# Kernel optimization log

Hardware: AMD Instinct MI355X
Metric: run time of the kernel (lower is better)

## Reference

```python
import jax, jax.numpy as jnp
import numpy as np

B, T, I, H, O = 64, 512, 64, 1024, 64
STEPS = 49 - 1  # output_len - 1 decode iterations


def _cell(x_t, h, c, Wih, Whh, b):
    # PyTorch LSTM gate order: i, f, g, o
    gates = x_t @ Wih.T + h @ Whh.T + b  # [B, 4H]
    i, f, g, o = jnp.split(gates, 4, axis=-1)
    i = jax.nn.sigmoid(i)
    f = jax.nn.sigmoid(f)
    g = jnp.tanh(g)
    o = jax.nn.sigmoid(o)
    c2 = f * c + i * g
    h2 = o * jnp.tanh(c2)
    return h2, c2


def setup_inputs() -> dict:
    key = jax.random.key(0)
    ks = jax.random.split(key, 12)
    s = 0.05
    return {
        "x": jax.random.normal(ks[0], (B, T, I), jnp.float32),
        "y0": jax.random.normal(ks[1], (B, I), jnp.float32),
        "Wih_e": jax.random.normal(ks[2], (4 * H, I), jnp.float32) * s,
        "Whh_e": jax.random.normal(ks[3], (4 * H, H), jnp.float32) * s,
        "bih_e": jax.random.normal(ks[4], (4 * H,), jnp.float32) * s,
        "bhh_e": jax.random.normal(ks[5], (4 * H,), jnp.float32) * s,
        "Wih_d": jax.random.normal(ks[6], (4 * H, I), jnp.float32) * s,
        "Whh_d": jax.random.normal(ks[7], (4 * H, H), jnp.float32) * s,
        "bih_d": jax.random.normal(ks[8], (4 * H,), jnp.float32) * s,
        "bhh_d": jax.random.normal(ks[9], (4 * H,), jnp.float32) * s,
        "Wfc": jax.random.normal(ks[10], (O, H), jnp.float32) * s,
        "bfc": jax.random.normal(ks[11], (O,), jnp.float32) * s,
    }


def reference(x, y0, Wih_e, Whh_e, bih_e, bhh_e, Wih_d, Whh_d, bih_d, bhh_d, Wfc, bfc):
    b = x.shape[0]
    h0 = jnp.zeros((b, Whh_e.shape[1]), x.dtype)
    c0 = h0

    # Encoder: scan over time (zero initial hidden, as in initHidden)
    be = bih_e + bhh_e

    def enc_step(carry, x_t):
        h, c = carry
        h, c = _cell(x_t, h, c, Wih_e, Whh_e, be)
        return (h, c), None

    (h, c), _ = jax.lax.scan(enc_step, (h0, c0), jnp.swapaxes(x, 0, 1))

    # Decoder: original loop never updates input_decoder -> constant y0 each step.
    bd = bih_d + bhh_d
    xin = y0 @ Wih_d.T + bd  # precompute constant input projection [B, 4H]

    def dec_step(carry, _):
        hd, cd = carry
        gates = xin + hd @ Whh_d.T
        i, f, g, o = jnp.split(gates, 4, axis=-1)
        i = jax.nn.sigmoid(i)
        f = jax.nn.sigmoid(f)
        g = jnp.tanh(g)
        o = jax.nn.sigmoid(o)
        c2 = f * cd + i * g
        h2 = o * jnp.tanh(c2)
        out = h2 @ Wfc.T + bfc  # [B, O]
        return (h2, c2), out

    _, ys = jax.lax.scan(dec_step, (h, c), None, length=STEPS)  # [STEPS, B, O]
    # torch.concat(total, dim=1): step-major along feature axis
    return jnp.swapaxes(ys, 0, 1).reshape(b, STEPS * ys.shape[-1])
```

## Files before the change

### kernel.cpp

```cpp
#include <hip/hip_runtime.h>
#include <hip/hip_fp16.h>

typedef _Float16 f16;
typedef _Float16 f16x8 __attribute__((ext_vector_type(8)));
typedef float f32x16 __attribute__((ext_vector_type(16)));

#define T_N 512
#define DSTEPS 48
#define TOTSTEPS 560
#define NWG 64

#define OFF_WHHE 0ull
#define SZ_WHH   (4096ull*1024*2)
#define OFF_WHHD (OFF_WHHE + SZ_WHH)
#define OFF_WIHE (OFF_WHHD + SZ_WHH)
#define SZ_WIH   (4096ull*64*2)
#define OFF_WIHD (OFF_WIHE + SZ_WIH)
#define OFF_WFC  (OFF_WIHD + SZ_WIH)
#define SZ_WFC   (64ull*1024*2)
#define OFF_XP   (OFF_WFC + SZ_WFC)
#define SZ_XP    (512ull*4096*2)
#define OFF_Y0   (OFF_XP + SZ_XP)
#define SZ_Y0    (4096ull*2)
#define OFF_BE   (OFF_Y0 + SZ_Y0)
#define OFF_BD   (OFF_BE + 4096ull*4)
#define OFF_FLG  (OFF_BD + 4096ull*4)
#define SZ_FLG   (561ull*256*4)
#define OFF_H    ((OFF_FLG + SZ_FLG + 255ull) & ~255ull)

__global__ void prologue(const float* __restrict__ x, const float* __restrict__ y0,
    const float* __restrict__ wihE, const float* __restrict__ whhE,
    const float* __restrict__ bihE, const float* __restrict__ bhhE,
    const float* __restrict__ wihD, const float* __restrict__ whhD,
    const float* __restrict__ bihD, const float* __restrict__ bhhD,
    const float* __restrict__ wfc, char* __restrict__ ws)
{
  const long long gid = (long long)blockIdx.x * 256 + threadIdx.x;
  const long long gsz = (long long)gridDim.x * 256;
  f16* whhEp = (f16*)(ws + OFF_WHHE);
  f16* whhDp = (f16*)(ws + OFF_WHHD);
  f16* wihEp = (f16*)(ws + OFF_WIHE);
  f16* wihDp = (f16*)(ws + OFF_WIHD);
  f16* wfcp  = (f16*)(ws + OFF_WFC);
  f16* xp    = (f16*)(ws + OFF_XP);
  f16* y0p   = (f16*)(ws + OFF_Y0);
  float* be  = (float*)(ws + OFF_BE);
  float* bd  = (float*)(ws + OFF_BD);

  for (long long idx = gid; idx < 4194304ll; idx += gsz) {
    int j = (int)idx & 7, l = (int)(idx >> 3) & 63, kk = (int)(idx >> 9) & 31;
    int i = (int)(idx >> 14) & 1, ks = (int)(idx >> 15) & 1, w = (int)(idx >> 16);
    int nl = i * 32 + (l & 31);
    int grow = (nl >> 4) * 1024 + w * 16 + (nl & 15);
    int k = ks * 512 + kk * 16 + ((l >> 5) << 3) + j;
    whhEp[idx] = (f16)whhE[(long long)grow * 1024 + k];
    whhDp[idx] = (f16)whhD[(long long)grow * 1024 + k];
  }
  for (long long idx = gid; idx < 262144ll; idx += gsz) {
    int j = (int)idx & 7, l = (int)(idx >> 3) & 63, kx = (int)(idx >> 9) & 1;
    int i = (int)(idx >> 10) & 1, ks = (int)(idx >> 11) & 1, w = (int)(idx >> 12);
    int nl = i * 32 + (l & 31);
    int grow = (nl >> 4) * 1024 + w * 16 + (nl & 15);
    int k = (ks * 2 + kx) * 16 + ((l >> 5) << 3) + j;
    wihEp[idx] = (f16)wihE[grow * 64 + k];
    wihDp[idx] = (f16)wihD[grow * 64 + k];
  }
  for (long long idx = gid; idx < 65536ll; idx += gsz) {
    int j = (int)idx & 7, l = (int)(idx >> 3) & 63, kk = (int)(idx >> 9) & 31;
    int i = (int)(idx >> 14) & 1, ks = (int)(idx >> 15) & 1;
    int o = i * 32 + (l & 31);
    int k = ks * 512 + kk * 16 + ((l >> 5) << 3) + j;
    wfcp[idx] = (f16)wfc[o * 1024 + k];
  }
  for (long long idx = gid; idx < 2097152ll; idx += gsz) {
    int kw = (int)idx & 15, b = (int)(idx >> 4) & 63, kkx = (int)(idx >> 10) & 3, t = (int)(idx >> 12);
    xp[idx] = (f16)x[(long long)b * 32768 + t * 64 + kkx * 16 + kw];
  }
  for (long long idx = gid; idx < 4096ll; idx += gsz) {
    int kw = (int)idx & 15, b = (int)(idx >> 4) & 63, kkx = (int)(idx >> 10) & 3;
    y0p[idx] = (f16)y0[b * 64 + kkx * 16 + kw];
  }
  for (long long idx = gid; idx < 4096ll; idx += gsz) {
    be[idx] = bihE[idx] + bhhE[idx];
    bd[idx] = bihD[idx] + bhhD[idx];
  }
}

__device__ __forceinline__ float sigf(float x) { return 1.0f / (1.0f + __expf(-x)); }
__device__ __forceinline__ float tanhfast(float x) {
  x = fminf(fmaxf(x, -15.f), 15.f);
  float e = __expf(2.0f * x);
  return (e - 1.0f) / (e + 1.0f);
}

#define MFMA(a,b,c) __builtin_amdgcn_mfma_f32_32x32x16_f16((a),(b),(c),0,0,0)

__launch_bounds__(256, 1)
__global__ void lstm_persist(char* __restrict__ ws, float* __restrict__ out,
                             const float* __restrict__ bfc)
{
  const int w    = blockIdx.x;
  const int tid  = threadIdx.x;
  const int lane = tid & 63;
  const int wave = tid >> 6;
  const int wm   = wave & 1;
  const int ks   = wave >> 1;

  const f16* whhEp = (const f16*)(ws + OFF_WHHE) + (size_t)w * 65536;
  const f16* whhDp = (const f16*)(ws + OFF_WHHD) + (size_t)w * 65536;
  const f16* wihEp = (const f16*)(ws + OFF_WIHE) + (size_t)w * 4096;
  const f16* wihDp = (const f16*)(ws + OFF_WIHD) + (size_t)w * 4096;
  const f16* wfcp  = (const f16*)(ws + OFF_WFC);
  const f16* xp    = (const f16*)(ws + OFF_XP);
  const f16* y0p   = (const f16*)(ws + OFF_Y0);
  const float* be  = (const float*)(ws + OFF_BE);
  const float* bd  = (const float*)(ws + OFF_BD);
  unsigned* flags  = (unsigned*)(ws + OFF_FLG);
  f16* hb          = (f16*)(ws + OFF_H);

  __shared__ float lds_g[2][64][66];
  __shared__ float bias_s[2][64];
  __shared__ unsigned seen[2];

  if (tid < 64) {
    int g4 = tid >> 4, u = tid & 15;
    bias_s[0][tid] = be[g4 * 1024 + w * 16 + u];
    bias_s[1][tid] = bd[g4 * 1024 + w * 16 + u];
  }
  if (tid < 2) seen[tid] = 0u;

  const int aoff = (wm * 32 + (lane & 31)) * 16 + (lane >> 5) * 8;
  const int boff = lane * 8;
  const int bsel = tid >> 2;
  const int u0   = (tid & 3) * 4;
  const int n0   = lane & 31;

  f16x8 bf0[32], bf1[32];
#pragma unroll
  for (int kk = 0; kk < 32; ++kk) {
    bf0[kk] = *(const f16x8*)(whhEp + (size_t)ks * 32768 + kk * 512 + boff);
    bf1[kk] = *(const f16x8*)(whhEp + (size_t)ks * 32768 + 16384 + kk * 512 + boff);
  }

  float c0 = 0.f, c1 = 0.f, c2 = 0.f, c3 = 0.f;
  __syncthreads();

#pragma unroll 1
  for (int t = 0; t < TOTSTEPS; ++t) {
    const bool enc = (t < T_N);

    if (t == T_N) {
#pragma unroll
      for (int kk = 0; kk < 32; ++kk) {
        bf0[kk] = *(const f16x8*)(whhDp + (size_t)ks * 32768 + kk * 512 + boff);
        bf1[kk] = *(const f16x8*)(whhDp + (size_t)ks * 32768 + 16384 + kk * 512 + boff);
      }
    }

    const f16* xblk = enc ? (xp + (size_t)t * 4096) : y0p;
    const f16* wihp = enc ? wihEp : wihDp;
    f16x8 xa0 = *(const f16x8*)(xblk + (ks * 2 + 0) * 1024 + aoff);
    f16x8 xa1 = *(const f16x8*)(xblk + (ks * 2 + 1) * 1024 + aoff);
    f16x8 wf0 = *(const f16x8*)(wihp + ((ks * 2 + 0) * 2 + 0) * 512 + boff);
    f16x8 wf1 = *(const f16x8*)(wihp + ((ks * 2 + 0) * 2 + 1) * 512 + boff);
    f16x8 wf2 = *(const f16x8*)(wihp + ((ks * 2 + 1) * 2 + 0) * 512 + boff);
    f16x8 wf3 = *(const f16x8*)(wihp + ((ks * 2 + 1) * 2 + 1) * 512 + boff);

    if (t > 0) {
      if (wave < 2) {
        const unsigned* fp = flags + (size_t)t * 256 + wave * 128 + lane;
        int ok;
        do {
          unsigned v0 = __hip_atomic_load(fp,      __ATOMIC_RELAXED, __HIP_MEMORY_SCOPE_AGENT);
          unsigned v1 = __hip_atomic_load(fp + 64, __ATOMIC_RELAXED, __HIP_MEMORY_SCOPE_AGENT);
          ok = __all((v0 == 1u) & (v1 == 1u));
          if (!ok) __builtin_amdgcn_s_sleep(1);
        } while (!ok);
        __hip_atomic_store(&seen[wave], (unsigned)t, __ATOMIC_RELEASE, __HIP_MEMORY_SCOPE_WORKGROUP);
      } else {
        while (__hip_atomic_load(&seen[wm], __ATOMIC_ACQUIRE, __HIP_MEMORY_SCOPE_WORKGROUP) < (unsigned)t)
          ;
      }
      asm volatile("" ::: "memory");
    }

    f16x8 af[32];
    if (t > 0) {
      const f16* hblk = hb + (size_t)(t - 1) * 65536;
#pragma unroll
      for (int kk = 0; kk < 32; ++kk)
        af[kk] = *(const f16x8*)(hblk + (size_t)(ks * 32 + kk) * 1024 + aoff);
    }

    f32x16 acc0, acc1;
#pragma unroll
    for (int i = 0; i < 16; ++i) { acc0[i] = 0.f; acc1[i] = 0.f; }
    acc0 = MFMA(xa0, wf0, acc0); acc0 = MFMA(xa1, wf1, acc0);
    acc1 = MFMA(xa0, wf2, acc1); acc1 = MFMA(xa1, wf3, acc1);

    if (t > 0) {
#pragma unroll
      for (int kk = 0; kk < 32; ++kk) {
        acc0 = MFMA(af[kk], bf0[kk], acc0);
        acc1 = MFMA(af[kk], bf1[kk], acc1);
      }
    }

    {
      const float* bs = enc ? bias_s[0] : bias_s[1];
      const float b0h = 0.5f * bs[n0];
      const float b1h = 0.5f * bs[32 + n0];
#pragma unroll
      for (int i = 0; i < 16; ++i) { acc0[i] += b0h; acc1[i] += b1h; }
    }

    {
      const int mb = wm * 32 + ((lane >> 5) << 2);
#pragma unroll
      for (int r = 0; r < 16; ++r) {
        const int m = mb + (r & 3) + ((r >> 2) << 3);
        lds_g[ks][n0][m]      = acc0[r];
        lds_g[ks][32 + n0][m] = acc1[r];
      }
    }
    __syncthreads();

    union { unsigned long long u64; f16 h4[4]; } hu;
    float cc[4] = {c0, c1, c2, c3};
#pragma unroll
    for (int j = 0; j < 4; ++j) {
      const int u = u0 + j;
      float ig = lds_g[0][u][bsel]      + lds_g[1][u][bsel];
      float fg = lds_g[0][16 + u][bsel] + lds_g[1][16 + u][bsel];
      float gg = lds_g[0][32 + u][bsel] + lds_g[1][32 + u][bsel];
      float og = lds_g[0][48 + u][bsel] + lds_g[1][48 + u][bsel];
      float cn = sigf(fg) * cc[j] + sigf(ig) * tanhfast(gg);
      cc[j] = cn;
      hu.h4[j] = (f16)(sigf(og) * tanhfast(cn));
    }
    c0 = cc[0]; c1 = cc[1]; c2 = cc[2]; c3 = cc[3];

    {
      f16* dst = hb + (size_t)t * 65536 + (size_t)w * 1024 + bsel * 16 + u0;
      unsigned long long addr = (unsigned long long)(size_t)dst;
      asm volatile("global_store_dwordx2 %0, %1, off sc0 sc1" : : "v"(addr), "v"(hu.u64) : "memory");
    }
    asm volatile("s_waitcnt vmcnt(0)" ::: "memory");
    if (lane == 0) {
      unsigned* fa = flags + (size_t)(t + 1) * 256 + wave * 64 + w;
      unsigned long long addr = (unsigned long long)(size_t)fa;
      unsigned one = 1u;
      asm volatile("global_store_dword %0, %1, off sc0 sc1" : : "v"(addr), "v"(one) : "memory");
    }
  }

  if (w < DSTEPS) {
    __syncthreads();
    const int s = T_N + 1 + w;
#pragma unroll
    for (int kk = 0; kk < 32; ++kk) {
      bf0[kk] = *(const f16x8*)(wfcp + (size_t)ks * 32768 + kk * 512 + boff);
      bf1[kk] = *(const f16x8*)(wfcp + (size_t)ks * 32768 + 16384 + kk * 512 + boff);
    }
    if (wave < 2) {
      const unsigned* fp = flags + (size_t)s * 256 + wave * 128 + lane;
      int ok;
      do {
        unsigned v0 = __hip_atomic_load(fp,      __ATOMIC_RELAXED, __HIP_MEMORY_SCOPE_AGENT);
        unsigned v1 = __hip_atomic_load(fp + 64, __ATOMIC_RELAXED, __HIP_MEMORY_SCOPE_AGENT);
        ok = __all((v0 == 1u) & (v1 == 1u));
        if (!ok) __builtin_amdgcn_s_sleep(1);
      } while (!ok);
      __hip_atomic_store(&seen[wave], (unsigned)s, __ATOMIC_RELEASE, __HIP_MEMORY_SCOPE_WORKGROUP);
    } else {
      while (__hip_atomic_load(&seen[wm], __ATOMIC_ACQUIRE, __HIP_MEMORY_SCOPE_WORKGROUP) < (unsigned)s)
        ;
    }
    asm volatile("" ::: "memory");

    const f16* hblk = hb + (size_t)(s - 1) * 65536;
    f16x8 af[32];
#pragma unroll
    for (int kk = 0; kk < 32; ++kk)
      af[kk] = *(const f16x8*)(hblk + (size_t)(ks * 32 + kk) * 1024 + aoff);

    f32x16 acc0, acc1;
#pragma unroll
    for (int i = 0; i < 16; ++i) { acc0[i] = 0.f; acc1[i] = 0.f; }
#pragma unroll
    for (int kk = 0; kk < 32; ++kk) {
      acc0 = MFMA(af[kk], bf0[kk], acc0);
      acc1 = MFMA(af[kk], bf1[kk], acc1);
    }
    {
      const int mb = wm * 32 + ((lane >> 5) << 2);
#pragma unroll
      for (int r = 0; r < 16; ++r) {
        const int m = mb + (r & 3) + ((r >> 2) << 3);
        lds_g[ks][n0][m]      = acc0[r];
        lds_g[ks][32 + n0][m] = acc1[r];
      }
    }
    __syncthreads();
    const int f0 = (tid & 3) * 16;
    float* op = out + (size_t)bsel * 3072 + w * 64 + f0;
#pragma unroll
    for (int c4 = 0; c4 < 4; ++c4) {
      float v4[4];
#pragma unroll
      for (int j = 0; j < 4; ++j) {
        const int f = f0 + c4 * 4 + j;
        v4[j] = lds_g[0][f][bsel] + lds_g[1][f][bsel] + bfc[f];
      }
      *(float4*)(op + c4 * 4) = make_float4(v4[0], v4[1], v4[2], v4[3]);
    }
  }
}

extern "C" void kernel_launch(void* const* d_in, const int* in_sizes, int n_in,
                              void* d_out, int out_size, void* d_ws, size_t ws_size,
                              hipStream_t stream) {
  const float* x    = (const float*)d_in[0];
  const float* y0   = (const float*)d_in[1];
  const float* wihE = (const float*)d_in[2];
  const float* whhE = (const float*)d_in[3];
  const float* bihE = (const float*)d_in[4];
  const float* bhhE = (const float*)d_in[5];
  const float* wihD = (const float*)d_in[6];
  const float* whhD = (const float*)d_in[7];
  const float* bihD = (const float*)d_in[8];
  const float* bhhD = (const float*)d_in[9];
  const float* wfc  = (const float*)d_in[10];
  const float* bfc  = (const float*)d_in[11];
  char* ws   = (char*)d_ws;
  float* out = (float*)d_out;

  prologue<<<256, 256, 0, stream>>>(x, y0, wihE, whhE, bihE, bhhE,
                                    wihD, whhD, bihD, bhhD, wfc, ws);
  lstm_persist<<<NWG, 256, 0, stream>>>(ws, out, bfc);
}
```

Measured before the change: 2.793 ms.

## Poll per-chunk producer flags in every wave and load h chunks as they arrive

Instead of two waves polling all 128 flags and relaying readiness through LDS, each wave now polls only the 32 producer flags covering its own K-slice. It issues the h-chunk loads incrementally as each producer's flag appears, so loads of early chunks overlap with waiting for late producers. A per-wave LDS step counter is added so a wave does not overwrite the lds_g gate buffer before its partner waves have finished reading the previous step. The new protocol relies on correct ordering of relaxed flag loads and data loads. The variable-mask unrolled load loop adds branching and can raise register pressure.

```diff
diff --git a/kernel.cpp b/kernel.cpp
--- a/kernel.cpp
+++ b/kernel.cpp
@@ -120,20 +120,22 @@
 
   __shared__ float lds_g[2][64][66];
   __shared__ float bias_s[2][64];
-  __shared__ unsigned seen[2];
+  __shared__ int   cellstep[4];
 
   if (tid < 64) {
     int g4 = tid >> 4, u = tid & 15;
     bias_s[0][tid] = be[g4 * 1024 + w * 16 + u];
     bias_s[1][tid] = bd[g4 * 1024 + w * 16 + u];
   }
-  if (tid < 2) seen[tid] = 0u;
+  if (tid < 4) cellstep[tid] = -1;
 
   const int aoff = (wm * 32 + (lane & 31)) * 16 + (lane >> 5) * 8;
   const int boff = lane * 8;
   const int bsel = tid >> 2;
   const int u0   = (tid & 3) * 4;
   const int n0   = lane & 31;
+
+  const unsigned foff = (unsigned)((2 * wm + (lane >> 5)) * 64 + 32 * ks + (lane & 31));
 
   f16x8 bf0[32], bf1[32];
 #pragma unroll
@@ -166,30 +168,26 @@
     f16x8 wf2 = *(const f16x8*)(wihp + ((ks * 2 + 1) * 2 + 0) * 512 + boff);
     f16x8 wf3 = *(const f16x8*)(wihp + ((ks * 2 + 1) * 2 + 1) * 512 + boff);
 
-    if (t > 0) {
-      if (wave < 2) {
-        const unsigned* fp = flags + (size_t)t * 256 + wave * 128 + lane;
-        int ok;
-        do {
-          unsigned v0 = __hip_atomic_load(fp,      __ATOMIC_RELAXED, __HIP_MEMORY_SCOPE_AGENT);
-          unsigned v1 = __hip_atomic_load(fp + 64, __ATOMIC_RELAXED, __HIP_MEMORY_SCOPE_AGENT);
-          ok = __all((v0 == 1u) & (v1 == 1u));
-          if (!ok) __builtin_amdgcn_s_sleep(1);
-        } while (!ok);
-        __hip_atomic_store(&seen[wave], (unsigned)t, __ATOMIC_RELEASE, __HIP_MEMORY_SCOPE_WORKGROUP);
-      } else {
-        while (__hip_atomic_load(&seen[wm], __ATOMIC_ACQUIRE, __HIP_MEMORY_SCOPE_WORKGROUP) < (unsigned)t)
-          ;
-      }
-      asm volatile("" ::: "memory");
-    }
-
     f16x8 af[32];
     if (t > 0) {
       const f16* hblk = hb + (size_t)(t - 1) * 65536;
-#pragma unroll
-      for (int kk = 0; kk < 32; ++kk)
-        af[kk] = *(const f16x8*)(hblk + (size_t)(ks * 32 + kk) * 1024 + aoff);
+      const unsigned* fb = flags + (size_t)t * 256 + foff;
+      unsigned done = 0u;
+      while (done != 0xFFFFFFFFu) {
+        unsigned v = __hip_atomic_load(fb, __ATOMIC_RELAXED, __HIP_MEMORY_SCOPE_AGENT);
+        unsigned long long b = __ballot(v == 1u);
+        unsigned ready = (unsigned)b & (unsigned)(b >> 32);
+        unsigned newly = ready & ~done;
+        if (newly) {
+#pragma unroll
+          for (int kk = 0; kk < 32; ++kk)
+            if (newly & (1u << kk))
+              af[kk] = *(const f16x8*)(hblk + (size_t)(ks * 32 + kk) * 1024 + aoff);
+          done |= newly;
+        } else {
+          __builtin_amdgcn_s_sleep(1);
+        }
+      }
     }
 
     f32x16 acc0, acc1;
@@ -212,6 +210,12 @@
       const float b1h = 0.5f * bs[32 + n0];
 #pragma unroll
       for (int i = 0; i < 16; ++i) { acc0[i] += b0h; acc1[i] += b1h; }
+    }
+
+    if (t > 0) {
+      while (__hip_atomic_load(&cellstep[2 * wm],     __ATOMIC_ACQUIRE, __HIP_MEMORY_SCOPE_WORKGROUP) < t - 1 ||
+             __hip_atomic_load(&cellstep[2 * wm + 1], __ATOMIC_ACQUIRE, __HIP_MEMORY_SCOPE_WORKGROUP) < t - 1)
+        ;
     }
 
     {
@@ -240,6 +244,8 @@
     }
     c0 = cc[0]; c1 = cc[1]; c2 = cc[2]; c3 = cc[3];
 
+    __hip_atomic_store(&cellstep[wave], t, __ATOMIC_RELEASE, __HIP_MEMORY_SCOPE_WORKGROUP);
+
     {
       f16* dst = hb + (size_t)t * 65536 + (size_t)w * 1024 + bsel * 16 + u0;
       unsigned long long addr = (unsigned long long)(size_t)dst;
@@ -262,21 +268,16 @@
       bf0[kk] = *(const f16x8*)(wfcp + (size_t)ks * 32768 + kk * 512 + boff);
       bf1[kk] = *(const f16x8*)(wfcp + (size_t)ks * 32768 + 16384 + kk * 512 + boff);
     }
-    if (wave < 2) {
-      const unsigned* fp = flags + (size_t)s * 256 + wave * 128 + lane;
+    {
+      const unsigned* fb = flags + (size_t)s * 256 + foff;
       int ok;
       do {
-        unsigned v0 = __hip_atomic_load(fp,      __ATOMIC_RELAXED, __HIP_MEMORY_SCOPE_AGENT);
-        unsigned v1 = __hip_atomic_load(fp + 64, __ATOMIC_RELAXED, __HIP_MEMORY_SCOPE_AGENT);
-        ok = __all((v0 == 1u) & (v1 == 1u));
+        unsigned v = __hip_atomic_load(fb, __ATOMIC_RELAXED, __HIP_MEMORY_SCOPE_AGENT);
+        ok = __all(v == 1u);
         if (!ok) __builtin_amdgcn_s_sleep(1);
       } while (!ok);
-      __hip_atomic_store(&seen[wave], (unsigned)s, __ATOMIC_RELEASE, __HIP_MEMORY_SCOPE_WORKGROUP);
-    } else {
-      while (__hip_atomic_load(&seen[wm], __ATOMIC_ACQUIRE, __HIP_MEMORY_SCOPE_WORKGROUP) < (unsigned)s)
-        ;
-    }
-    asm volatile("" ::: "memory");
+      asm volatile("" ::: "memory");
+    }
 
     const f16* hblk = hb + (size_t)(s - 1) * 65536;
     f16x8 af[32];
```

Result: slower. 5.229 ms (+87.2%).
